# Kernel optimization log

Measured on AMD Instinct MI355X. Metric: run time of the kernel, lower is better.

Reference implementation:

```python
import jax, jax.numpy as jnp
import numpy as np

GROUPS = 2
STRIDE = (1, 1)
PADDING = ((1, 1), (1, 1))
DILATION = (1, 1)


def setup_inputs() -> dict:
    key = jax.random.key(0)
    k1, k2, k3 = jax.random.split(key, 3)
    B, Cin, H, W = 16, 256, 112, 112
    Cout, kH, kW = 256, 3, 3
    x = jax.random.normal(k1, (B, Cin, H, W), dtype=jnp.float32)
    # kaiming_uniform-like scale: fan_in = (Cin/groups)*kH*kW
    fan_in = (Cin // GROUPS) * kH * kW
    bound = float(np.sqrt(1.0 / fan_in))
    weight = jax.random.uniform(k2, (Cout, Cin // GROUPS, kH, kW), dtype=jnp.float32,
                                minval=-bound, maxval=bound)
    bias = jax.random.uniform(k3, (Cout,), dtype=jnp.float32, minval=-bound, maxval=bound)
    return {"x": x, "weight": weight, "bias": bias}


def reference(x, weight, bias):
    # Grouped conv2d: every backend path of SparseGroupedConv2d (sparse triton
    # active-tile kernel, zero-tile skip, dense F.conv2d fallback) computes this
    # exact grouped convolution; the tile machinery only skips zero-energy tiles.
    y = jax.lax.conv_general_dilated(
        x, weight,
        window_strides=STRIDE,
        padding=PADDING,
        rhs_dilation=DILATION,
        dimension_numbers=("NCHW", "OIHW", "NCHW"),
        feature_group_count=GROUPS,
    )
    return y + bias[None, :, None, None]
```

## Files before the change

### kernel.cpp

```cpp
#include <hip/hip_runtime.h>
#include <hip/hip_bf16.h>
#include <stdint.h>

#define BATCH 16
#define CIN   256
#define HH    112
#define WW    112
#define GROUPS 2
#define CG    128
#define COG   128
#define CK    32
#define NCHUNK (CG/CK)

typedef __bf16 bf16x8 __attribute__((ext_vector_type(8)));
typedef float  f32x4  __attribute__((ext_vector_type(4)));

#define WB_BYTES   (GROUPS*3*3*COG*CG*2)
#define ZBUF_OFF   WB_BYTES
#define ZBUF_BYTES 8192
#define XB_OFF     (ZBUF_OFF + ZBUF_BYTES)
#define XB_BYTES   ((size_t)BATCH*HH*WW*CIN*2)
#define WS_NEED    ((size_t)XB_OFF + XB_BYTES)

__device__ inline void load_lds16(const void* g, void* l) {
    __builtin_amdgcn_global_load_lds(
        (const __attribute__((address_space(1))) void*)g,
        (__attribute__((address_space(3))) void*)l, 16, 0, 0);
}

__global__ __launch_bounds__(256) void k_wcvt(const float* __restrict__ w,
                                              ushort* __restrict__ wb) {
    int i = blockIdx.x * 256 + threadIdx.x;
    int ci = i & 127;
    int t  = i >> 7;
    int co = t & 127;
    t >>= 7;
    int kw = t % 3; t /= 3;
    int kh = t % 3;
    int g  = t / 3;
    int src = (((g*COG + co)*CG + ci)*3 + kh)*3 + kw;
    __hip_bfloat16 v = __float2bfloat16(w[src]);
    wb[i] = *reinterpret_cast<ushort*>(&v);
}

#define XPAD 113
__global__ __launch_bounds__(256) void k_xcvt(const float* __restrict__ x,
                                              ushort* __restrict__ xb) {
    __shared__ float tile[64 * XPAD];
    int bid = blockIdx.x;
    int cc  = bid & 3;
    int h   = (bid >> 2) % HH;
    int b   = bid / (4 * HH);
    int tid = threadIdx.x;

    const float* src = x + ((size_t)(b*CIN + cc*64) * HH + h) * WW;
    for (int tt = tid; tt < 64*28; tt += 256) {
        int c = tt / 28, v = tt % 28;
        float4 f = *reinterpret_cast<const float4*>(src + (size_t)c*HH*WW + v*4);
        float* d = &tile[c*XPAD + v*4];
        d[0]=f.x; d[1]=f.y; d[2]=f.z; d[3]=f.w;
    }
    __syncthreads();

    if (tid < 224) {
        int w = tid >> 1, half = tid & 1;
        ushort o[32];
#pragma unroll
        for (int j = 0; j < 32; ++j) {
            __hip_bfloat16 v = __float2bfloat16(tile[(half*32 + j)*XPAD + w]);
            o[j] = *reinterpret_cast<ushort*>(&v);
        }
        ushort* dst = xb + (((size_t)(b*HH + h)*WW + w)*CIN + cc*64 + half*32);
        const uint4* o4 = reinterpret_cast<const uint4*>(o);
        uint4* d4 = reinterpret_cast<uint4*>(dst);
        d4[0]=o4[0]; d4[1]=o4[1]; d4[2]=o4[2]; d4[3]=o4[3];
    }
}

__device__ inline void stage_w3(const ushort* __restrict__ wb, ushort* dstbuf,
                                int g, int tap_base, int cin, int wave, int lane) {
    int co = wave*16 + (lane >> 2);
    int ts = (lane & 3) ^ ((lane >> 3) & 3);
#pragma unroll
    for (int i = 0; i < 3; ++i) {
        const ushort* src = wb + (((size_t)(g*9 + tap_base + i)*COG + co)*CG + cin + ts*8);
        load_lds16(src, dstbuf + (i*COG + wave*16)*CK);
    }
}

__device__ inline void xpre_task(const ushort* __restrict__ xb, ushort* dstbuf,
                                 const ushort* __restrict__ zbuf,
                                 int b, int g, int oh0n, int cin, int t, int lane) {
    int rr = t / 7, ii = t % 7;
    int h  = oh0n - 1 + rr;
    int qv = lane >> 2;
    int w_in = ii*16 + qv;
    int ts = (lane & 3) ^ (((2*rr + 1 + qv) >> 1) & 3);
    const ushort* src = (h >= 0 && h < HH)
        ? xb + (((size_t)(b*HH + h)*WW + w_in)*CIN + g*CG + cin + ts*8)
        : zbuf + lane*8;
    load_lds16(src, dstbuf + (rr*114 + 1 + ii*16)*CK);
}

#define PHASE(KH, KW, XCUR, WBUF)                                           \
  {                                                                         \
    int sB = lk ^ (((2*(wr + (KH)) + l15 + (KW)) >> 1) & 3);                \
    const ushort* bbase = (XCUR) + ((wr + (KH))*114 + l15 + (KW))*CK + sB*8;\
    bf16x8 bfr[7];                                                          \
    _Pragma("unroll")                                                       \
    for (int n = 0; n < 7; ++n)                                             \
      bfr[n] = *reinterpret_cast<const bf16x8*>(bbase + n*16*CK);           \
    const ushort* abase = (WBUF) + ((KW)*COG + wm*32 + l15)*CK + sA*8;      \
    __builtin_amdgcn_s_setprio(1);                                          \
    _Pragma("unroll")                                                       \
    for (int m = 0; m < 2; ++m) {                                           \
      bf16x8 afr = *reinterpret_cast<const bf16x8*>(abase + m*16*CK);       \
      _Pragma("unroll")                                                     \
      for (int n = 0; n < 7; ++n)                                           \
        acc[m][n] = __builtin_amdgcn_mfma_f32_16x16x32_bf16(                \
            afr, bfr[n], acc[m][n], 0, 0, 0);                               \
    }                                                                       \
    __builtin_amdgcn_s_setprio(0);                                          \
  }

#define GROUP3(KH, XCUR, WBUF)   \
    PHASE(KH, 0, XCUR, WBUF)     \
    PHASE(KH, 1, XCUR, WBUF)     \
    PHASE(KH, 2, XCUR, WBUF)

__global__ __launch_bounds__(512, 2) void k_conv(const ushort* __restrict__ xb,
                                                 const ushort* __restrict__ wb,
                                                 const float* __restrict__ bias,
                                                 float* __restrict__ out,
                                                 const ushort* __restrict__ zbuf) {
    __shared__ __align__(16) ushort xs[2][4*114*CK];
    __shared__ __align__(16) ushort wsb[2][3*COG*CK];

    int g    = blockIdx.x >> 7;
    int rem  = blockIdx.x & 127;
    int b    = rem >> 3;
    int q0   = (rem & 7) * 7;

    int tid  = threadIdx.x;
    int wave = tid >> 6;
    int lane = tid & 63;
    int wm   = wave >> 1;
    int wr   = wave & 1;
    int l15  = lane & 15;
    int lk   = lane >> 4;
    int sA   = lk ^ ((l15 >> 1) & 3);

    {
        int buf = tid >> 8, r2 = (tid >> 6) & 3, wc = (tid >> 5) & 1, ch = tid & 31;
        xs[buf][(r2*114 + wc*113)*CK + ch] = 0;
    }

    float breg[2][4];
#pragma unroll
    for (int m = 0; m < 2; ++m)
#pragma unroll
        for (int j = 0; j < 4; ++j)
            breg[m][j] = bias[g*COG + wm*32 + m*16 + lk*4 + j];

    f32x4 acc[2][7];
#pragma unroll
    for (int m = 0; m < 2; ++m)
#pragma unroll
        for (int n = 0; n < 7; ++n) acc[m][n] = f32x4{0.f,0.f,0.f,0.f};

    for (int t = wave; t < 28; t += 8)
        xpre_task(xb, xs[0], zbuf, b, g, 2*q0, 0, t, lane);
    stage_w3(wb, wsb[0], g, 0, 0, wave, lane);
    __syncthreads();

#pragma unroll 1
    for (int CC = 0; CC < 28; ++CC) {
        int e    = CC >> 2;
        int oh0  = 2*(q0 + e);
        int p0   = CC & 1;
        const ushort* xcur = xs[p0];
        int cin  = (CC & 3) * CK;
        int cinN = ((CC + 1) & 3) * CK;
        int oh0n = 2*(q0 + ((CC + 1) >> 2));

        stage_w3(wb, wsb[p0^1], g, 3, cin, wave, lane);
        if (CC < 27) {
            xpre_task(xb, xs[p0^1], zbuf, b, g, oh0n, cinN, wave,     lane);
            xpre_task(xb, xs[p0^1], zbuf, b, g, oh0n, cinN, wave + 8, lane);
        }
        GROUP3(0, xcur, wsb[p0])
        __syncthreads();

        stage_w3(wb, wsb[p0], g, 6, cin, wave, lane);
        if (CC < 27) {
            xpre_task(xb, xs[p0^1], zbuf, b, g, oh0n, cinN, wave + 16, lane);
            if (wave + 24 < 28)
                xpre_task(xb, xs[p0^1], zbuf, b, g, oh0n, cinN, wave + 24, lane);
        }
        GROUP3(1, xcur, wsb[p0^1])
        __syncthreads();

        if (CC < 27)
            stage_w3(wb, wsb[p0^1], g, 0, cinN, wave, lane);
        GROUP3(2, xcur, wsb[p0])
        __syncthreads();

        if ((CC & 3) == 3) {
            int oh = oh0 + wr;
#pragma unroll
            for (int m = 0; m < 2; ++m) {
                int co = g*COG + wm*32 + m*16 + lk*4;
#pragma unroll
                for (int j = 0; j < 4; ++j) {
                    float bv = breg[m][j];
                    float* orow = out + (((size_t)(b*CIN + co + j)*HH + oh)*WW);
#pragma unroll
                    for (int n = 0; n < 7; ++n)
                        orow[n*16 + l15] = acc[m][n][j] + bv;
                }
            }
#pragma unroll
            for (int m = 0; m < 2; ++m)
#pragma unroll
                for (int n = 0; n < 7; ++n) acc[m][n] = f32x4{0.f,0.f,0.f,0.f};
        }
    }
}

__global__ __launch_bounds__(128) void k_direct(const float* __restrict__ x,
                                                const float* __restrict__ w,
                                                const float* __restrict__ bias,
                                                float* __restrict__ out) {
    int bid = blockIdx.x;
    int oh  = bid % HH;
    int t   = bid / HH;
    int co  = t % CIN;
    int b   = t / CIN;
    int ow  = threadIdx.x;
    if (ow >= WW) return;
    int g = co / COG;
    float s = bias[co];
    const float* wp = w + (size_t)co*CG*9;
    const float* xp = x + ((size_t)b*CIN + g*CG)*HH*WW;
    for (int ci = 0; ci < CG; ++ci) {
        const float* xr = xp + (size_t)ci*HH*WW;
        const float* wr_ = wp + ci*9;
#pragma unroll
        for (int kh = 0; kh < 3; ++kh) {
            int ih = oh + kh - 1;
            if (ih < 0 || ih >= HH) continue;
#pragma unroll
            for (int kw = 0; kw < 3; ++kw) {
                int iw = ow + kw - 1;
                if (iw < 0 || iw >= WW) continue;
                s += xr[ih*WW + iw] * wr_[kh*3 + kw];
            }
        }
    }
    out[(((size_t)b*CIN + co)*HH + oh)*WW + ow] = s;
}

extern "C" void kernel_launch(void* const* d_in, const int* in_sizes, int n_in,
                              void* d_out, int out_size, void* d_ws, size_t ws_size,
                              hipStream_t stream) {
    const float* x    = (const float*)d_in[0];
    const float* w    = (const float*)d_in[1];
    const float* bias = (const float*)d_in[2];
    float* out        = (float*)d_out;

    if (ws_size >= WS_NEED) {
        ushort* wb   = (ushort*)d_ws;
        ushort* zb   = (ushort*)((char*)d_ws + ZBUF_OFF);
        ushort* xbuf = (ushort*)((char*)d_ws + XB_OFF);
        hipMemsetAsync(zb, 0, ZBUF_BYTES, stream);
        k_wcvt<<<1152, 256, 0, stream>>>(w, wb);
        k_xcvt<<<BATCH*HH*4, 256, 0, stream>>>(x, xbuf);
        k_conv<<<256, 512, 0, stream>>>(xbuf, wb, bias, out, zb);
    } else {
        k_direct<<<BATCH*CIN*HH, 128, 0, stream>>>(x, w, bias, out);
    }
}
```

Before: 226.4 us.

## Enlarge per-wave output tile to 64 channels by 4 rows with fragment prefetch

Each wave now computes 4 output rows by 64 channels, so each block covers 16 output rows and the grid shrinks to 224 blocks. The LDS input tile grows to 6 rows. A and B fragments are double-buffered in registers so the next kernel column's LDS loads overlap the current MFMAs. This is meant to raise MFMA work per LDS read and hide LDS latency, at the cost of more registers, more LDS and fewer blocks than CUs can host.

```diff
diff --git a/kernel.cpp b/kernel.cpp
--- a/kernel.cpp
+++ b/kernel.cpp
@@ -10,7 +10,7 @@
 #define CG    128
 #define COG   128
 #define CK    32
-#define NCHUNK (CG/CK)
+#define RH    4
 
 typedef __bf16 bf16x8 __attribute__((ext_vector_type(8)));
 typedef float  f32x4  __attribute__((ext_vector_type(4)));
@@ -102,125 +102,130 @@
     load_lds16(src, dstbuf + (rr*114 + 1 + ii*16)*CK);
 }
 
-#define PHASE(KH, KW, XCUR, WBUF)                                           \
+#define LOADF(P, KH, KW, XCUR, WBUF)                                        \
   {                                                                         \
     int sB = lk ^ (((2*(wr + (KH)) + l15 + (KW)) >> 1) & 3);                \
     const ushort* bbase = (XCUR) + ((wr + (KH))*114 + l15 + (KW))*CK + sB*8;\
-    bf16x8 bfr[7];                                                          \
     _Pragma("unroll")                                                       \
     for (int n = 0; n < 7; ++n)                                             \
-      bfr[n] = *reinterpret_cast<const bf16x8*>(bbase + n*16*CK);           \
-    const ushort* abase = (WBUF) + ((KW)*COG + wm*32 + l15)*CK + sA*8;      \
+      Bf[P][n] = *reinterpret_cast<const bf16x8*>(bbase + n*16*CK);         \
+    const ushort* abase = (WBUF) + ((KW)*COG + wm*64 + l15)*CK + sA*8;      \
+    _Pragma("unroll")                                                       \
+    for (int m = 0; m < 4; ++m)                                             \
+      Af[P][m] = *reinterpret_cast<const bf16x8*>(abase + m*16*CK);         \
+  }
+
+#define MFMAF(P)                                                            \
     __builtin_amdgcn_s_setprio(1);                                          \
     _Pragma("unroll")                                                       \
-    for (int m = 0; m < 2; ++m) {                                           \
-      bf16x8 afr = *reinterpret_cast<const bf16x8*>(abase + m*16*CK);       \
+    for (int m = 0; m < 4; ++m)                                             \
       _Pragma("unroll")                                                     \
       for (int n = 0; n < 7; ++n)                                           \
         acc[m][n] = __builtin_amdgcn_mfma_f32_16x16x32_bf16(                \
-            afr, bfr[n], acc[m][n], 0, 0, 0);                               \
-    }                                                                       \
-    __builtin_amdgcn_s_setprio(0);                                          \
-  }
-
-#define GROUP3(KH, XCUR, WBUF)   \
-    PHASE(KH, 0, XCUR, WBUF)     \
-    PHASE(KH, 1, XCUR, WBUF)     \
-    PHASE(KH, 2, XCUR, WBUF)
+            Af[P][m], Bf[P][n], acc[m][n], 0, 0, 0);                        \
+    __builtin_amdgcn_s_setprio(0);
 
 __global__ __launch_bounds__(512, 2) void k_conv(const ushort* __restrict__ xb,
                                                  const ushort* __restrict__ wb,
                                                  const float* __restrict__ bias,
                                                  float* __restrict__ out,
                                                  const ushort* __restrict__ zbuf) {
-    __shared__ __align__(16) ushort xs[2][4*114*CK];
+    __shared__ __align__(16) ushort xs[2][6*114*CK];
     __shared__ __align__(16) ushort wsb[2][3*COG*CK];
 
-    int g    = blockIdx.x >> 7;
-    int rem  = blockIdx.x & 127;
-    int b    = rem >> 3;
-    int q0   = (rem & 7) * 7;
+    int g   = blockIdx.x / 112;
+    int rem = blockIdx.x % 112;
+    int b   = rem / 7;
+    int qb  = rem % 7;
 
     int tid  = threadIdx.x;
     int wave = tid >> 6;
     int lane = tid & 63;
-    int wm   = wave >> 1;
-    int wr   = wave & 1;
+    int wm   = wave >> 2;
+    int wr   = wave & 3;
     int l15  = lane & 15;
     int lk   = lane >> 4;
     int sA   = lk ^ ((l15 >> 1) & 3);
 
-    {
-        int buf = tid >> 8, r2 = (tid >> 6) & 3, wc = (tid >> 5) & 1, ch = tid & 31;
-        xs[buf][(r2*114 + wc*113)*CK + ch] = 0;
-    }
-
-    float breg[2][4];
-#pragma unroll
-    for (int m = 0; m < 2; ++m)
-#pragma unroll
-        for (int j = 0; j < 4; ++j)
-            breg[m][j] = bias[g*COG + wm*32 + m*16 + lk*4 + j];
-
-    f32x4 acc[2][7];
-#pragma unroll
-    for (int m = 0; m < 2; ++m)
+    for (int t = tid; t < 768; t += 512) {
+        int buf = t / 384, r2 = t % 384;
+        int rr = r2 / 64, wc = (r2 >> 5) & 1, ch = r2 & 31;
+        xs[buf][(rr*114 + wc*113)*CK + ch] = 0;
+    }
+
+    bf16x8 Af[2][4], Bf[2][7];
+    f32x4 acc[4][7];
+#pragma unroll
+    for (int m = 0; m < 4; ++m)
 #pragma unroll
         for (int n = 0; n < 7; ++n) acc[m][n] = f32x4{0.f,0.f,0.f,0.f};
 
-    for (int t = wave; t < 28; t += 8)
-        xpre_task(xb, xs[0], zbuf, b, g, 2*q0, 0, t, lane);
+    for (int t = wave; t < 42; t += 8)
+        xpre_task(xb, xs[0], zbuf, b, g, qb*16, 0, t, lane);
     stage_w3(wb, wsb[0], g, 0, 0, wave, lane);
     __syncthreads();
 
 #pragma unroll 1
-    for (int CC = 0; CC < 28; ++CC) {
+    for (int CC = 0; CC < 16; ++CC) {
         int e    = CC >> 2;
-        int oh0  = 2*(q0 + e);
+        int oh0  = qb*16 + e*4;
         int p0   = CC & 1;
         const ushort* xcur = xs[p0];
         int cin  = (CC & 3) * CK;
         int cinN = ((CC + 1) & 3) * CK;
-        int oh0n = 2*(q0 + ((CC + 1) >> 2));
-
+        int oh0n = qb*16 + ((CC + 1) >> 2) * 4;
+
+        LOADF(0, 0, 0, xcur, wsb[p0])
+        LOADF(1, 0, 1, xcur, wsb[p0])
         stage_w3(wb, wsb[p0^1], g, 3, cin, wave, lane);
-        if (CC < 27) {
-            xpre_task(xb, xs[p0^1], zbuf, b, g, oh0n, cinN, wave,     lane);
-            xpre_task(xb, xs[p0^1], zbuf, b, g, oh0n, cinN, wave + 8, lane);
-        }
-        GROUP3(0, xcur, wsb[p0])
+        if (CC < 15)
+            for (int t = wave; t < 21; t += 8)
+                xpre_task(xb, xs[p0^1], zbuf, b, g, oh0n, cinN, t, lane);
+        MFMAF(0)
+        LOADF(0, 0, 2, xcur, wsb[p0])
+        MFMAF(1)
+        MFMAF(0)
         __syncthreads();
 
+        LOADF(0, 1, 0, xcur, wsb[p0^1])
+        LOADF(1, 1, 1, xcur, wsb[p0^1])
         stage_w3(wb, wsb[p0], g, 6, cin, wave, lane);
-        if (CC < 27) {
-            xpre_task(xb, xs[p0^1], zbuf, b, g, oh0n, cinN, wave + 16, lane);
-            if (wave + 24 < 28)
-                xpre_task(xb, xs[p0^1], zbuf, b, g, oh0n, cinN, wave + 24, lane);
-        }
-        GROUP3(1, xcur, wsb[p0^1])
+        if (CC < 15)
+            for (int t = 21 + wave; t < 42; t += 8)
+                xpre_task(xb, xs[p0^1], zbuf, b, g, oh0n, cinN, t, lane);
+        MFMAF(0)
+        LOADF(0, 1, 2, xcur, wsb[p0^1])
+        MFMAF(1)
+        MFMAF(0)
         __syncthreads();
 
-        if (CC < 27)
+        LOADF(0, 2, 0, xcur, wsb[p0])
+        LOADF(1, 2, 1, xcur, wsb[p0])
+        if (CC < 15)
             stage_w3(wb, wsb[p0^1], g, 0, cinN, wave, lane);
-        GROUP3(2, xcur, wsb[p0])
+        MFMAF(0)
+        LOADF(0, 2, 2, xcur, wsb[p0])
+        MFMAF(1)
+        MFMAF(0)
         __syncthreads();
 
         if ((CC & 3) == 3) {
             int oh = oh0 + wr;
 #pragma unroll
-            for (int m = 0; m < 2; ++m) {
-                int co = g*COG + wm*32 + m*16 + lk*4;
+            for (int m = 0; m < 4; ++m) {
+                int cob = g*COG + wm*64 + m*16 + lk*4;
 #pragma unroll
                 for (int j = 0; j < 4; ++j) {
-                    float bv = breg[m][j];
-                    float* orow = out + (((size_t)(b*CIN + co + j)*HH + oh)*WW);
+                    int co = cob + j;
+                    float bv = bias[co];
+                    float* orow = out + (((size_t)(b*CIN + co)*HH + oh)*WW);
 #pragma unroll
                     for (int n = 0; n < 7; ++n)
                         orow[n*16 + l15] = acc[m][n][j] + bv;
                 }
             }
 #pragma unroll
-            for (int m = 0; m < 2; ++m)
+            for (int m = 0; m < 4; ++m)
 #pragma unroll
                 for (int n = 0; n < 7; ++n) acc[m][n] = f32x4{0.f,0.f,0.f,0.f};
         }
@@ -275,7 +280,7 @@
         hipMemsetAsync(zb, 0, ZBUF_BYTES, stream);
         k_wcvt<<<1152, 256, 0, stream>>>(w, wb);
         k_xcvt<<<BATCH*HH*4, 256, 0, stream>>>(x, xbuf);
-        k_conv<<<256, 512, 0, stream>>>(xbuf, wb, bias, out, zb);
+        k_conv<<<224, 512, 0, stream>>>(xbuf, wb, bias, out, zb);
     } else {
         k_direct<<<BATCH*CIN*HH, 128, 0, stream>>>(x, w, bias, out);
     }
```

New measurement: 300.9 us. 1.33x slower.
